# Kernel tuning notes

Hardware: AMD Instinct MI355X
Metric: run time of the kernel (lower is better)

The kernel has to match this reference:

```python
import jax, jax.numpy as jnp
import numpy as np
import math

IMAGE_SIZE = 256
VIEWING_ANGLE = 30.0  # degrees
NEAR = 0.1
FAR = 100.0
CHUNK = 50


def _look_at(vertices):
    # nr.look_at with at=origin, up=+y, eye from viewing_angle (as in __init__)
    eye = jnp.array([0.0, 0.0, -(1.0 / math.tan(math.radians(VIEWING_ANGLE)) + 1.0)],
                    dtype=vertices.dtype)
    at = jnp.zeros(3, dtype=vertices.dtype)
    up = jnp.array([0.0, 1.0, 0.0], dtype=vertices.dtype)
    z = at - eye
    z = z / jnp.linalg.norm(z)
    x = jnp.cross(up, z)
    x = x / jnp.linalg.norm(x)
    y = jnp.cross(z, x)
    y = y / jnp.linalg.norm(y)
    R = jnp.stack([x, y, z])  # [3,3] rows = camera axes
    return (vertices - eye) @ R.T


def _perspective(v):
    # nr.perspective: x,y divided by z*tan(angle); z (camera depth) kept
    width = math.tan(math.radians(VIEWING_ANGLE))
    z = v[..., 2]
    zs = jnp.where(jnp.abs(z) < 1e-5, 1e-5, z)  # avoid div-by-zero for behind-camera verts
    return jnp.stack([v[..., 0] / (zs * width), v[..., 1] / (zs * width), z], axis=-1)


def reference(vertices, faces):
    """Renderer.forward(vertices, faces, mode='depth'):
    fill_back -> look_at -> perspective -> vertices_to_faces -> rasterize_depth.
    Returns depth image [B, H, W] (FAR where no face covers the pixel)."""
    B = vertices.shape[0]
    # fill_back: append faces with reversed vertex order
    faces2 = jnp.concatenate([faces, faces[:, :, ::-1]], axis=1)  # [B, 2F, 3]
    v_scr = _perspective(_look_at(vertices))                      # [B, V, 3]
    # vertices_to_faces gather
    fv = jax.vmap(lambda v, f: v[f])(v_scr, faces2)               # [B, 2F, 3, 3]
    F2 = fv.shape[1]
    nsteps = F2 // CHUNK
    fv = fv.reshape(B, nsteps, CHUNK, 3, 3).transpose(1, 0, 2, 3, 4)  # [S,B,C,3,3]

    is_ = IMAGE_SIZE
    p = (2.0 * jnp.arange(is_, dtype=vertices.dtype) + 1.0 - is_) / is_  # pixel centers in (-1,1)
    py, px = jnp.meshgrid(p, p, indexing='ij')  # [H,W]

    def step(buf, f):  # f: [B,C,3,3]; z-buffer min over this face chunk
        x = f[..., 0][..., None, None]  # [B,C,3,1,1]
        y = f[..., 1][..., None, None]
        z = f[..., 2]                   # [B,C,3] camera-space depth per vertex
        x0, x1, x2 = x[:, :, 0], x[:, :, 1], x[:, :, 2]
        y0, y1, y2 = y[:, :, 0], y[:, :, 1], y[:, :, 2]
        area = (x1 - x0) * (y2 - y0) - (x2 - x0) * (y1 - y0)  # [B,C,1,1] signed 2*area
        area_s = jnp.where(jnp.abs(area) < 1e-8, 1e-8, area)
        # screen-space barycentric weights (edge functions / area)
        w0 = ((x1 - px) * (y2 - py) - (x2 - px) * (y1 - py)) / area_s
        w1 = ((x2 - px) * (y0 - py) - (x0 - px) * (y2 - py)) / area_s
        w2 = 1.0 - w0 - w1
        zc = jnp.maximum(z, 1e-4)  # safe for masked-out faces only
        # perspective-correct depth: z = 1 / (w0/z0 + w1/z1 + w2/z2)
        inv_z = (w0 / zc[:, :, 0, None, None] + w1 / zc[:, :, 1, None, None]
                 + w2 / zc[:, :, 2, None, None])
        zp = 1.0 / jnp.maximum(inv_z, 1e-6)
        front = jnp.all(z > NEAR, axis=-1)[..., None, None]
        inside = (w0 >= 0) & (w1 >= 0) & (w2 >= 0) & (jnp.abs(area) > 1e-8)
        valid = inside & front & (zp > NEAR) & (zp < FAR)
        zp = jnp.where(valid, zp, FAR)
        return jnp.minimum(buf, jnp.min(zp, axis=1)), None

    buf0 = jnp.full((B, is_, is_), FAR, dtype=vertices.dtype)
    depth, _ = jax.lax.scan(step, buf0, fv)
    return depth


def setup_inputs() -> dict:
    key = jax.random.key(0)
    kv, kf = jax.random.split(key)
    B, NV, NF = 1, 2502, 5000
    # mesh roughly within the camera frustum (eye at z~-2.73 looking at origin)
    vertices = 0.35 * jax.random.normal(kv, (B, NV, 3), dtype=jnp.float32)
    faces = jax.random.randint(kf, (B, NF, 3), 0, NV, dtype=jnp.int32)
    return {"vertices": vertices, "faces": faces}
```

## Files before the change

### kernel.cpp

```cpp
#include <hip/hip_runtime.h>
#include <hip/hip_bf16.h>

#define IS 256
#define NEARV 0.1f
#define FARV 100.0f
#define NTX 16
#define NTILES 256
#define CAP 5120
#define CHK 32
#define BINTH 128
#define RBLOCKS 2048
#define RWAVES (RBLOCKS * 4)
#define MAXITEMS (NTILES * ((CAP + CHK - 1) / CHK))

__global__ void kprep(const float* __restrict__ verts, const int* __restrict__ faces,
                      float4* __restrict__ fd, unsigned int* __restrict__ zb,
                      int* __restrict__ count, int* __restrict__ nitems, int nf) {
    int i = blockIdx.x * 256 + threadIdx.x;
    zb[i] = 0x42C80000u;
    if (i < NTILES) count[i] = 0;
    if (i == NTILES) *nitems = 0;
    if (i >= nf) return;
    int i0 = faces[i * 3 + 0];
    int i1 = faces[i * 3 + 1];
    int i2 = faces[i * 3 + 2];
    float z0 = verts[i0 * 3 + 2] + 2.7320508075688772f;
    float z1 = verts[i1 * 3 + 2] + 2.7320508075688772f;
    float z2 = verts[i2 * 3 + 2] + 2.7320508075688772f;
    bool front = (z0 > NEARV) && (z1 > NEARV) && (z2 > NEARV);
    float zs0 = (fabsf(z0) < 1e-5f) ? 1e-5f : z0;
    float zs1 = (fabsf(z1) < 1e-5f) ? 1e-5f : z1;
    float zs2 = (fabsf(z2) < 1e-5f) ? 1e-5f : z2;
    float d0 = zs0 * 0.57735026918962576f;
    float d1 = zs1 * 0.57735026918962576f;
    float d2 = zs2 * 0.57735026918962576f;
    float x0 = verts[i0 * 3 + 0] / d0;
    float y0 = verts[i0 * 3 + 1] / d0;
    float x1 = verts[i1 * 3 + 0] / d1;
    float y1 = verts[i1 * 3 + 1] / d1;
    float x2 = verts[i2 * 3 + 0] / d2;
    float y2 = verts[i2 * 3 + 1] / d2;
    float area = (x1 - x0) * (y2 - y0) - (x2 - x0) * (y1 - y0);
    float4* o = fd + (size_t)i * 4;
    if (front && (fabsf(area) > 1e-8f)) {
        float xmin = fminf(x0, fminf(x1, x2));
        float xmax = fmaxf(x0, fmaxf(x1, x2));
        float ymin = fminf(y0, fminf(y1, y2));
        float ymax = fmaxf(y0, fmaxf(y1, y2));
        float ia = 1.0f / area;
        float iz0 = 1.0f / fmaxf(z0, 1e-4f);
        float iz1 = 1.0f / fmaxf(z1, 1e-4f);
        float iz2 = 1.0f / fmaxf(z2, 1e-4f);
        o[0] = make_float4(x0, y0, x1, y1);
        o[1] = make_float4(x2, y2, ia, iz0);
        o[2] = make_float4(iz1, iz2, 0.0f, 0.0f);
        o[3] = make_float4(xmin, ymin, xmax, ymax);
    } else {
        o[3] = make_float4(3.0e8f, 3.0e8f, -3.0e8f, -3.0e8f);
    }
}

__global__ void kbin(const float4* __restrict__ fd, int* __restrict__ count,
                     unsigned short* __restrict__ list, int nf) {
    __shared__ int scnt[NTILES];
    __shared__ int sbase[NTILES];
    const int tid = threadIdx.x;
    for (int t = tid; t < NTILES; t += BINTH) scnt[t] = 0;
    __syncthreads();
    const int f = blockIdx.x * BINTH + tid;
    int kx0 = 0, kx1 = -1, ky0 = 0, ky1 = -1;
    float4 bb = make_float4(0.f, 0.f, 0.f, 0.f);
    if (f < nf) {
        bb = fd[(size_t)f * 4 + 3];
        float tminx = fminf(fmaxf((bb.x * 256.0f + 225.0f) * (1.0f / 32.0f), -2.0f), 17.0f);
        float tmaxx = fminf(fmaxf((bb.z * 256.0f + 255.0f) * (1.0f / 32.0f), -2.0f), 17.0f);
        float tminy = fminf(fmaxf((bb.y * 256.0f + 225.0f) * (1.0f / 32.0f), -2.0f), 17.0f);
        float tmaxy = fminf(fmaxf((bb.w * 256.0f + 255.0f) * (1.0f / 32.0f), -2.0f), 17.0f);
        kx0 = max(0, (int)ceilf(tminx) - 1);
        kx1 = min(NTX - 1, (int)floorf(tmaxx) + 1);
        ky0 = max(0, (int)ceilf(tminy) - 1);
        ky1 = min(NTX - 1, (int)floorf(tmaxy) + 1);
    }
    for (int ky = ky0; ky <= ky1; ++ky) {
        float py_lo = (float)(32 * ky - 255) * (1.0f / 256.0f);
        float py_hi = (float)(32 * ky - 225) * (1.0f / 256.0f);
        if (!(bb.y <= py_hi && bb.w >= py_lo)) continue;
        for (int kx = kx0; kx <= kx1; ++kx) {
            float px_lo = (float)(32 * kx - 255) * (1.0f / 256.0f);
            float px_hi = (float)(32 * kx - 225) * (1.0f / 256.0f);
            if (bb.x <= px_hi && bb.z >= px_lo) atomicAdd(&scnt[ky * NTX + kx], 1);
        }
    }
    __syncthreads();
    for (int t = tid; t < NTILES; t += BINTH) {
        int c = scnt[t];
        sbase[t] = (c > 0) ? atomicAdd(&count[t], c) : 0;
        scnt[t] = 0;
    }
    __syncthreads();
    for (int ky = ky0; ky <= ky1; ++ky) {
        float py_lo = (float)(32 * ky - 255) * (1.0f / 256.0f);
        float py_hi = (float)(32 * ky - 225) * (1.0f / 256.0f);
        if (!(bb.y <= py_hi && bb.w >= py_lo)) continue;
        for (int kx = kx0; kx <= kx1; ++kx) {
            float px_lo = (float)(32 * kx - 255) * (1.0f / 256.0f);
            float px_hi = (float)(32 * kx - 225) * (1.0f / 256.0f);
            if (bb.x <= px_hi && bb.z >= px_lo) {
                int t = ky * NTX + kx;
                int slot = sbase[t] + atomicAdd(&scnt[t], 1);
                list[(size_t)t * CAP + slot] = (unsigned short)f;
            }
        }
    }
}

__global__ void kitems(const int* __restrict__ count, int* __restrict__ items,
                       int* __restrict__ nitems) {
    __shared__ int snch[NTILES];
    __shared__ int soff[NTILES];
    const int t = threadIdx.x;
    int c = count[t];
    snch[t] = (c + CHK - 1) / CHK;
    __syncthreads();
    if (t == 0) {
        int run = 0;
        for (int i = 0; i < NTILES; ++i) { soff[i] = run; run += snch[i]; }
        *nitems = run;
    }
    __syncthreads();
    int off = soff[t];
    int n = snch[t];
    for (int k = 0; k < n; ++k) items[off + k] = (t << 16) | k;
}

__launch_bounds__(256)
__global__ void kraster(const float4* __restrict__ fd, const unsigned short* __restrict__ list,
                        const int* __restrict__ count, const int* __restrict__ items,
                        const int* __restrict__ nitems, unsigned int* __restrict__ zb) {
    const int wid = blockIdx.x * 4 + (threadIdx.x >> 6);
    const int lane = threadIdx.x & 63;
    const int cx = lane & 15;
    const int ry = lane >> 4;
    const int ni = *nitems;

    for (int it = wid; it < ni; it += RWAVES) {
        const int pk = items[it];
        const int tile = pk >> 16;
        const int chunk = pk & 0xffff;
        const int bx = tile & 15;
        const int by = tile >> 4;
        const int j = bx * 16 + cx;
        const float px = ((float)(2 * j + 1) - 256.0f) * (1.0f / 256.0f);
        float py[4];
        int row[4];
#pragma unroll
        for (int r = 0; r < 4; ++r) {
            row[r] = by * 16 + ry + 4 * r;
            py[r] = ((float)(2 * row[r] + 1) - 256.0f) * (1.0f / 256.0f);
        }
        const int s = chunk * CHK;
        const int n = min(CHK, count[tile] - s);
        const unsigned short* lp = list + (size_t)tile * CAP + s;

        float mx[4] = {0.0f, 0.0f, 0.0f, 0.0f};

#pragma unroll 2
        for (int e = 0; e < n; ++e) {
            const int fidx = lp[e];
            const float4* p = fd + (size_t)fidx * 4;
            float4 a0 = p[0];
            float4 a1 = p[1];
            float4 a2 = p[2];
            float dx0 = a0.x - px, dx1 = a0.z - px, dx2 = a1.x - px;
#pragma unroll
            for (int r = 0; r < 4; ++r) {
                float dy0 = a0.y - py[r], dy1 = a0.w - py[r], dy2 = a1.y - py[r];
                float e0 = dx1 * dy2 - dx2 * dy1;
                float e1 = dx2 * dy0 - dx0 * dy2;
                float w0 = e0 * a1.z;
                float w1 = e1 * a1.z;
                float w2 = 1.0f - w0 - w1;
                float invz = w0 * a1.w + w1 * a2.x + w2 * a2.y;
                float invzc = fmaxf(invz, 1e-6f);
                bool ok = (w0 >= 0.0f) && (w1 >= 0.0f) && (w2 >= 0.0f) &&
                          (invzc < 10.0f) && (invzc > 0.01f);
                if (ok) mx[r] = fmaxf(mx[r], invzc);
            }
        }
#pragma unroll
        for (int r = 0; r < 4; ++r) {
            if (mx[r] > 0.0f) {
                float zp = 1.0f / mx[r];
                atomicMin(&zb[row[r] * IS + j], __float_as_uint(zp));
            }
        }
    }
}

extern "C" void kernel_launch(void* const* d_in, const int* in_sizes, int n_in,
                              void* d_out, int out_size, void* d_ws, size_t ws_size,
                              hipStream_t stream) {
    const float* verts = (const float*)d_in[0];
    const int* faces = (const int*)d_in[1];
    unsigned int* zb = (unsigned int*)d_out;

    const int nf = in_sizes[1] / 3;

    char* ws = (char*)d_ws;
    size_t off = 0;
    float4* fd = (float4*)(ws + off);            off += (size_t)nf * 64;
    off = (off + 255) & ~(size_t)255;
    int* count = (int*)(ws + off);               off += NTILES * 4;
    off = (off + 255) & ~(size_t)255;
    int* nitems = (int*)(ws + off);              off += 256;
    int* items = (int*)(ws + off);               off += (size_t)MAXITEMS * 4;
    off = (off + 255) & ~(size_t)255;
    unsigned short* list = (unsigned short*)(ws + off);

    kprep<<<(IS * IS) / 256, 256, 0, stream>>>(verts, faces, fd, zb, count, nitems, nf);
    kbin<<<(nf + BINTH - 1) / BINTH, BINTH, 0, stream>>>(fd, count, list, nf);
    kitems<<<1, 256, 0, stream>>>(count, items, nitems);
    kraster<<<RBLOCKS, 256, 0, stream>>>(fd, list, count, items, nitems, zb);
}
```

Measured before the change: 109.4 us.

## Fuse face prep with binning, fold item build into last block, trim raster atomics

Face projection is merged into the binning kernel, so bounding boxes no longer round-trip through memory. The separate single-block item-list kernel is replaced by a last-block-done pattern that runs a parallel prefix scan, which removes one launch. Raster waves now read the chunk length from the packed item, load face indices two at a time as wave-uniform scalars, and skip the atomicMin when the pre-read depth already beats the candidate. This adds a grid-wide atomic counter with threadfences and a more complex item encoding.

```diff
diff --git a/kernel.cpp b/kernel.cpp
--- a/kernel.cpp
+++ b/kernel.cpp
@@ -8,91 +8,91 @@
 #define NTILES 256
 #define CAP 5120
 #define CHK 32
-#define BINTH 128
+#define CPT ((CAP + CHK - 1) / CHK)
 #define RBLOCKS 2048
 #define RWAVES (RBLOCKS * 4)
-#define MAXITEMS (NTILES * ((CAP + CHK - 1) / CHK))
-
-__global__ void kprep(const float* __restrict__ verts, const int* __restrict__ faces,
-                      float4* __restrict__ fd, unsigned int* __restrict__ zb,
-                      int* __restrict__ count, int* __restrict__ nitems, int nf) {
+#define MAXITEMS (NTILES * CPT)
+
+__global__ void kinit(unsigned int* __restrict__ zb, int* __restrict__ count,
+                      int* __restrict__ misc) {
     int i = blockIdx.x * 256 + threadIdx.x;
     zb[i] = 0x42C80000u;
     if (i < NTILES) count[i] = 0;
-    if (i == NTILES) *nitems = 0;
-    if (i >= nf) return;
-    int i0 = faces[i * 3 + 0];
-    int i1 = faces[i * 3 + 1];
-    int i2 = faces[i * 3 + 2];
-    float z0 = verts[i0 * 3 + 2] + 2.7320508075688772f;
-    float z1 = verts[i1 * 3 + 2] + 2.7320508075688772f;
-    float z2 = verts[i2 * 3 + 2] + 2.7320508075688772f;
-    bool front = (z0 > NEARV) && (z1 > NEARV) && (z2 > NEARV);
-    float zs0 = (fabsf(z0) < 1e-5f) ? 1e-5f : z0;
-    float zs1 = (fabsf(z1) < 1e-5f) ? 1e-5f : z1;
-    float zs2 = (fabsf(z2) < 1e-5f) ? 1e-5f : z2;
-    float d0 = zs0 * 0.57735026918962576f;
-    float d1 = zs1 * 0.57735026918962576f;
-    float d2 = zs2 * 0.57735026918962576f;
-    float x0 = verts[i0 * 3 + 0] / d0;
-    float y0 = verts[i0 * 3 + 1] / d0;
-    float x1 = verts[i1 * 3 + 0] / d1;
-    float y1 = verts[i1 * 3 + 1] / d1;
-    float x2 = verts[i2 * 3 + 0] / d2;
-    float y2 = verts[i2 * 3 + 1] / d2;
-    float area = (x1 - x0) * (y2 - y0) - (x2 - x0) * (y1 - y0);
-    float4* o = fd + (size_t)i * 4;
-    if (front && (fabsf(area) > 1e-8f)) {
-        float xmin = fminf(x0, fminf(x1, x2));
-        float xmax = fmaxf(x0, fmaxf(x1, x2));
-        float ymin = fminf(y0, fminf(y1, y2));
-        float ymax = fmaxf(y0, fmaxf(y1, y2));
-        float ia = 1.0f / area;
-        float iz0 = 1.0f / fmaxf(z0, 1e-4f);
-        float iz1 = 1.0f / fmaxf(z1, 1e-4f);
-        float iz2 = 1.0f / fmaxf(z2, 1e-4f);
-        o[0] = make_float4(x0, y0, x1, y1);
-        o[1] = make_float4(x2, y2, ia, iz0);
-        o[2] = make_float4(iz1, iz2, 0.0f, 0.0f);
-        o[3] = make_float4(xmin, ymin, xmax, ymax);
-    } else {
-        o[3] = make_float4(3.0e8f, 3.0e8f, -3.0e8f, -3.0e8f);
-    }
-}
-
-__global__ void kbin(const float4* __restrict__ fd, int* __restrict__ count,
-                     unsigned short* __restrict__ list, int nf) {
+    if (i == NTILES) misc[0] = 0;
+}
+
+__launch_bounds__(256)
+__global__ void kbinprep(const float* __restrict__ verts, const int* __restrict__ faces,
+                         float4* __restrict__ fd, int* __restrict__ count,
+                         unsigned short* __restrict__ list, int* __restrict__ misc,
+                         int* __restrict__ items, int nf) {
     __shared__ int scnt[NTILES];
     __shared__ int sbase[NTILES];
+    __shared__ int slast;
     const int tid = threadIdx.x;
-    for (int t = tid; t < NTILES; t += BINTH) scnt[t] = 0;
-    __syncthreads();
-    const int f = blockIdx.x * BINTH + tid;
+    for (int t = tid; t < NTILES; t += 256) scnt[t] = 0;
+    __syncthreads();
+
+    const int f = blockIdx.x * 256 + tid;
     int kx0 = 0, kx1 = -1, ky0 = 0, ky1 = -1;
-    float4 bb = make_float4(0.f, 0.f, 0.f, 0.f);
+    float bxmin = 0.f, bymin = 0.f, bxmax = -1.f, bymax = -1.f;
     if (f < nf) {
-        bb = fd[(size_t)f * 4 + 3];
-        float tminx = fminf(fmaxf((bb.x * 256.0f + 225.0f) * (1.0f / 32.0f), -2.0f), 17.0f);
-        float tmaxx = fminf(fmaxf((bb.z * 256.0f + 255.0f) * (1.0f / 32.0f), -2.0f), 17.0f);
-        float tminy = fminf(fmaxf((bb.y * 256.0f + 225.0f) * (1.0f / 32.0f), -2.0f), 17.0f);
-        float tmaxy = fminf(fmaxf((bb.w * 256.0f + 255.0f) * (1.0f / 32.0f), -2.0f), 17.0f);
-        kx0 = max(0, (int)ceilf(tminx) - 1);
-        kx1 = min(NTX - 1, (int)floorf(tmaxx) + 1);
-        ky0 = max(0, (int)ceilf(tminy) - 1);
-        ky1 = min(NTX - 1, (int)floorf(tmaxy) + 1);
+        int i0 = faces[f * 3 + 0];
+        int i1 = faces[f * 3 + 1];
+        int i2 = faces[f * 3 + 2];
+        float z0 = verts[i0 * 3 + 2] + 2.7320508075688772f;
+        float z1 = verts[i1 * 3 + 2] + 2.7320508075688772f;
+        float z2 = verts[i2 * 3 + 2] + 2.7320508075688772f;
+        bool front = (z0 > NEARV) && (z1 > NEARV) && (z2 > NEARV);
+        float zs0 = (fabsf(z0) < 1e-5f) ? 1e-5f : z0;
+        float zs1 = (fabsf(z1) < 1e-5f) ? 1e-5f : z1;
+        float zs2 = (fabsf(z2) < 1e-5f) ? 1e-5f : z2;
+        float d0 = zs0 * 0.57735026918962576f;
+        float d1 = zs1 * 0.57735026918962576f;
+        float d2 = zs2 * 0.57735026918962576f;
+        float x0 = verts[i0 * 3 + 0] / d0;
+        float y0 = verts[i0 * 3 + 1] / d0;
+        float x1 = verts[i1 * 3 + 0] / d1;
+        float y1 = verts[i1 * 3 + 1] / d1;
+        float x2 = verts[i2 * 3 + 0] / d2;
+        float y2 = verts[i2 * 3 + 1] / d2;
+        float area = (x1 - x0) * (y2 - y0) - (x2 - x0) * (y1 - y0);
+        if (front && (fabsf(area) > 1e-8f)) {
+            float xmin = fminf(x0, fminf(x1, x2));
+            float xmax = fmaxf(x0, fmaxf(x1, x2));
+            float ymin = fminf(y0, fminf(y1, y2));
+            float ymax = fmaxf(y0, fmaxf(y1, y2));
+            float ia = 1.0f / area;
+            float iz0 = 1.0f / fmaxf(z0, 1e-4f);
+            float iz1 = 1.0f / fmaxf(z1, 1e-4f);
+            float iz2 = 1.0f / fmaxf(z2, 1e-4f);
+            float4* o = fd + (size_t)f * 4;
+            o[0] = make_float4(x0, y0, x1, y1);
+            o[1] = make_float4(x2, y2, ia, iz0);
+            o[2] = make_float4(iz1, iz2, 0.0f, 0.0f);
+            bxmin = xmin; bymin = ymin; bxmax = xmax; bymax = ymax;
+            float tminx = fminf(fmaxf((bxmin * 256.0f + 225.0f) * (1.0f / 32.0f), -2.0f), 17.0f);
+            float tmaxx = fminf(fmaxf((bxmax * 256.0f + 255.0f) * (1.0f / 32.0f), -2.0f), 17.0f);
+            float tminy = fminf(fmaxf((bymin * 256.0f + 225.0f) * (1.0f / 32.0f), -2.0f), 17.0f);
+            float tmaxy = fminf(fmaxf((bymax * 256.0f + 255.0f) * (1.0f / 32.0f), -2.0f), 17.0f);
+            kx0 = max(0, (int)ceilf(tminx) - 1);
+            kx1 = min(NTX - 1, (int)floorf(tmaxx) + 1);
+            ky0 = max(0, (int)ceilf(tminy) - 1);
+            ky1 = min(NTX - 1, (int)floorf(tmaxy) + 1);
+        }
     }
     for (int ky = ky0; ky <= ky1; ++ky) {
         float py_lo = (float)(32 * ky - 255) * (1.0f / 256.0f);
         float py_hi = (float)(32 * ky - 225) * (1.0f / 256.0f);
-        if (!(bb.y <= py_hi && bb.w >= py_lo)) continue;
+        if (!(bymin <= py_hi && bymax >= py_lo)) continue;
         for (int kx = kx0; kx <= kx1; ++kx) {
             float px_lo = (float)(32 * kx - 255) * (1.0f / 256.0f);
             float px_hi = (float)(32 * kx - 225) * (1.0f / 256.0f);
-            if (bb.x <= px_hi && bb.z >= px_lo) atomicAdd(&scnt[ky * NTX + kx], 1);
-        }
-    }
-    __syncthreads();
-    for (int t = tid; t < NTILES; t += BINTH) {
+            if (bxmin <= px_hi && bxmax >= px_lo) atomicAdd(&scnt[ky * NTX + kx], 1);
+        }
+    }
+    __syncthreads();
+    for (int t = tid; t < NTILES; t += 256) {
         int c = scnt[t];
         sbase[t] = (c > 0) ? atomicAdd(&count[t], c) : 0;
         scnt[t] = 0;
@@ -101,72 +101,80 @@
     for (int ky = ky0; ky <= ky1; ++ky) {
         float py_lo = (float)(32 * ky - 255) * (1.0f / 256.0f);
         float py_hi = (float)(32 * ky - 225) * (1.0f / 256.0f);
-        if (!(bb.y <= py_hi && bb.w >= py_lo)) continue;
+        if (!(bymin <= py_hi && bymax >= py_lo)) continue;
         for (int kx = kx0; kx <= kx1; ++kx) {
             float px_lo = (float)(32 * kx - 255) * (1.0f / 256.0f);
             float px_hi = (float)(32 * kx - 225) * (1.0f / 256.0f);
-            if (bb.x <= px_hi && bb.z >= px_lo) {
+            if (bxmin <= px_hi && bxmax >= px_lo) {
                 int t = ky * NTX + kx;
                 int slot = sbase[t] + atomicAdd(&scnt[t], 1);
                 list[(size_t)t * CAP + slot] = (unsigned short)f;
             }
         }
     }
-}
-
-__global__ void kitems(const int* __restrict__ count, int* __restrict__ items,
-                       int* __restrict__ nitems) {
-    __shared__ int snch[NTILES];
-    __shared__ int soff[NTILES];
-    const int t = threadIdx.x;
-    int c = count[t];
-    snch[t] = (c + CHK - 1) / CHK;
-    __syncthreads();
-    if (t == 0) {
-        int run = 0;
-        for (int i = 0; i < NTILES; ++i) { soff[i] = run; run += snch[i]; }
-        *nitems = run;
-    }
-    __syncthreads();
-    int off = soff[t];
-    int n = snch[t];
-    for (int k = 0; k < n; ++k) items[off + k] = (t << 16) | k;
+    __syncthreads();
+    __threadfence();
+    if (tid == 0) slast = (atomicAdd(&misc[0], 1) == (int)gridDim.x - 1) ? 1 : 0;
+    __syncthreads();
+    if (!slast) return;
+    __threadfence();
+    int c = __hip_atomic_load(&count[tid], __ATOMIC_RELAXED, __HIP_MEMORY_SCOPE_AGENT);
+    int nch = (c + CHK - 1) / CHK;
+    scnt[tid] = nch;
+    __syncthreads();
+    for (int d = 1; d < NTILES; d <<= 1) {
+        int v = (tid >= d) ? scnt[tid - d] : 0;
+        __syncthreads();
+        scnt[tid] += v;
+        __syncthreads();
+    }
+    int off = scnt[tid] - nch;
+    if (tid == NTILES - 1) misc[64] = scnt[tid];
+    for (int k = 0; k < nch; ++k) {
+        int n = min(CHK, c - k * CHK);
+        items[off + k] = (tid << 16) | (n << 8) | k;
+    }
 }
 
 __launch_bounds__(256)
-__global__ void kraster(const float4* __restrict__ fd, const unsigned short* __restrict__ list,
-                        const int* __restrict__ count, const int* __restrict__ items,
-                        const int* __restrict__ nitems, unsigned int* __restrict__ zb) {
-    const int wid = blockIdx.x * 4 + (threadIdx.x >> 6);
+__global__ void kraster(const float4* __restrict__ fd, const unsigned int* __restrict__ list32,
+                        const int* __restrict__ items, const int* __restrict__ misc,
+                        unsigned int* __restrict__ zb) {
+    const int wslot = __builtin_amdgcn_readfirstlane(threadIdx.x >> 6);
+    const int wid = blockIdx.x * 4 + wslot;
     const int lane = threadIdx.x & 63;
     const int cx = lane & 15;
     const int ry = lane >> 4;
-    const int ni = *nitems;
+    const int ni = __builtin_amdgcn_readfirstlane(misc[64]);
 
     for (int it = wid; it < ni; it += RWAVES) {
-        const int pk = items[it];
+        const int pk = __builtin_amdgcn_readfirstlane(items[it]);
         const int tile = pk >> 16;
-        const int chunk = pk & 0xffff;
+        const int n = (pk >> 8) & 0xff;
+        const int chunk = pk & 0xff;
         const int bx = tile & 15;
         const int by = tile >> 4;
         const int j = bx * 16 + cx;
         const float px = ((float)(2 * j + 1) - 256.0f) * (1.0f / 256.0f);
         float py[4];
         int row[4];
+        unsigned int zcur[4];
 #pragma unroll
         for (int r = 0; r < 4; ++r) {
             row[r] = by * 16 + ry + 4 * r;
             py[r] = ((float)(2 * row[r] + 1) - 256.0f) * (1.0f / 256.0f);
-        }
-        const int s = chunk * CHK;
-        const int n = min(CHK, count[tile] - s);
-        const unsigned short* lp = list + (size_t)tile * CAP + s;
+            zcur[r] = zb[row[r] * IS + j];
+        }
+        const unsigned int* lp32 = list32 + ((size_t)tile * CAP + chunk * CHK) / 2;
 
         float mx[4] = {0.0f, 0.0f, 0.0f, 0.0f};
+        unsigned int pr = 0;
 
 #pragma unroll 2
         for (int e = 0; e < n; ++e) {
-            const int fidx = lp[e];
+            if ((e & 1) == 0)
+                pr = (unsigned int)__builtin_amdgcn_readfirstlane((int)lp32[e >> 1]);
+            const int fidx = (e & 1) ? (int)(pr >> 16) : (int)(pr & 0xffffu);
             const float4* p = fd + (size_t)fidx * 4;
             float4 a0 = p[0];
             float4 a1 = p[1];
@@ -182,8 +190,8 @@
                 float w2 = 1.0f - w0 - w1;
                 float invz = w0 * a1.w + w1 * a2.x + w2 * a2.y;
                 float invzc = fmaxf(invz, 1e-6f);
-                bool ok = (w0 >= 0.0f) && (w1 >= 0.0f) && (w2 >= 0.0f) &&
-                          (invzc < 10.0f) && (invzc > 0.01f);
+                float wmin = fminf(fminf(w0, w1), w2);
+                bool ok = (wmin >= 0.0f) && (invzc < 10.0f) && (invzc > 0.01f);
                 if (ok) mx[r] = fmaxf(mx[r], invzc);
             }
         }
@@ -191,7 +199,8 @@
         for (int r = 0; r < 4; ++r) {
             if (mx[r] > 0.0f) {
                 float zp = 1.0f / mx[r];
-                atomicMin(&zb[row[r] * IS + j], __float_as_uint(zp));
+                unsigned int zbits = __float_as_uint(zp);
+                if (zbits < zcur[r]) atomicMin(&zb[row[r] * IS + j], zbits);
             }
         }
     }
@@ -212,13 +221,14 @@
     off = (off + 255) & ~(size_t)255;
     int* count = (int*)(ws + off);               off += NTILES * 4;
     off = (off + 255) & ~(size_t)255;
-    int* nitems = (int*)(ws + off);              off += 256;
+    int* misc = (int*)(ws + off);                off += 512;
     int* items = (int*)(ws + off);               off += (size_t)MAXITEMS * 4;
     off = (off + 255) & ~(size_t)255;
     unsigned short* list = (unsigned short*)(ws + off);
 
-    kprep<<<(IS * IS) / 256, 256, 0, stream>>>(verts, faces, fd, zb, count, nitems, nf);
-    kbin<<<(nf + BINTH - 1) / BINTH, BINTH, 0, stream>>>(fd, count, list, nf);
-    kitems<<<1, 256, 0, stream>>>(count, items, nitems);
-    kraster<<<RBLOCKS, 256, 0, stream>>>(fd, list, count, items, nitems, zb);
-}
+    const int nb = (nf + 255) / 256;
+
+    kinit<<<(IS * IS) / 256, 256, 0, stream>>>(zb, count, misc);
+    kbinprep<<<nb, 256, 0, stream>>>(verts, faces, fd, count, list, misc, items, nf);
+    kraster<<<RBLOCKS, 256, 0, stream>>>(fd, (const unsigned int*)list, items, misc, zb);
+}
```

New measurement: 110.9 us. Within noise of the previous version (+1.4%).
